# Optimization experiments

Measured on AMD Instinct MI355X. Metric: run time of the kernel, lower is better.

## Reference

```python
import jax, jax.numpy as jnp
import numpy as np

N_IN, N_REC, N_OUT = 512, 2048, 128
D_MAX = 4      # delays drawn from [0, D_MAX]; possible_delays = 1..D_MAX
DT = 0.001


@jax.custom_vjp
def spike(v):
    # SpikeFunc.forward: heaviside(v > 0)
    return (v > 0.0).astype(v.dtype)

def _spike_fwd(v):
    return spike(v), v

def _spike_bwd(v, g):
    # SpikeFunc.backward: grad passes through unchanged for v >= 0,
    # scaled by relu(1 + v) for v < 0
    return (g * jnp.where(v < 0.0, jnp.maximum(1.0 + v, 0.0), 1.0),)

spike.defvjp(_spike_fwd, _spike_bwd)


def setup_inputs() -> dict:
    key = jax.random.key(0)
    ks = jax.random.split(key, 6)
    B, T = 64, 250
    x = (jax.random.uniform(ks[0], (B, N_IN, T)) < 0.05).astype(jnp.float32)
    delays = jax.random.randint(ks[1], (N_REC, N_REC), 0, D_MAX + 1, dtype=jnp.int32)

    def kaiming_uniform(k, shape, fan):
        bound = float(np.sqrt(6.0 / fan))
        return jax.random.uniform(k, shape, minval=-bound, maxval=bound, dtype=jnp.float32)

    W_i = kaiming_uniform(ks[2], (N_REC, N_IN), N_REC)            # fan_out mode
    W_r = kaiming_uniform(ks[3], (N_REC, N_REC), N_REC) * 0.05    # scaled for stable dynamics
    W_o = kaiming_uniform(ks[4], (N_OUT, N_REC), N_REC)
    return {
        'input_spike_raster': x,
        'delays': delays,
        'W_i': W_i, 'W_r': W_r, 'W_o': W_o,
        'B_r': jnp.zeros((N_REC,), jnp.float32),
        'B_o': jnp.zeros((N_OUT,), jnp.float32),
        'tau_rec': jnp.full((1,), 0.2, jnp.float32),
        'tau_out': jnp.full((1,), 0.2, jnp.float32),
        'thr_rec': jnp.full((1,), 0.5, jnp.float32),
    }


def reference(input_spike_raster, delays, W_i, W_r, W_o, B_r, B_o, tau_rec, tau_out, thr_rec):
    rec_c = jnp.exp(-DT * 10.0 / tau_rec)   # (1,)
    out_c = jnp.exp(-DT * 10.0 / tau_out)   # (1,)
    d_vals = jnp.arange(1, D_MAX + 1)       # possible (nonzero) delays
    # W_r * delay_mask.T for each delay d -> (D, n_rec, n_rec)
    masks = (delays[None, :, :] == d_vals[:, None, None])
    Wd = W_r[None] * jnp.transpose(masks, (0, 2, 1)).astype(W_r.dtype)

    B, n_in, T = input_spike_raster.shape
    xs = jnp.transpose(input_spike_raster, (2, 0, 1))  # (T, B, n_in)
    buf0 = jnp.zeros((D_MAX, B, N_REC), W_r.dtype)     # buf[k] = spikes at t-1-k

    def step(carry, inp):
        mem_rec, mem_out, buf = carry
        t, x_t = inp
        cur = x_t @ W_i.T + B_r                               # (B, n_rec)
        # delay d contributes only if t > d (matches torch `if t > d`)
        valid = (t > d_vals).astype(cur.dtype)                # (D,)
        cur = cur + jnp.einsum('dbn,dmn->bm', buf * valid[:, None, None], Wd)
        mem_rec = mem_rec * rec_c + cur
        z = spike(mem_rec - thr_rec)
        mem_rec = mem_rec - z * thr_rec
        mem_out = mem_out * out_c + z @ W_o.T + B_o
        buf = jnp.concatenate([z[None], buf[:-1]], axis=0)
        return (mem_rec, mem_out, buf), z

    init = (jnp.zeros((B, N_REC), W_r.dtype), jnp.zeros((B, N_OUT), W_r.dtype), buf0)
    (_, mem_out, _), zs = jax.lax.scan(step, init, (jnp.arange(T), xs))
    # torch returns (mem_pot_out, stack(rec_spikes, dim=2)) -> (B, n_rec, T)
    return mem_out, jnp.transpose(zs, (1, 2, 0))
```

## Files before the change

kernel.cpp:

```cpp
#include <hip/hip_runtime.h>

#define NIN  512
#define NREC 2048
#define NOUT 128
#define BB   64
#define TT   250

#define OFF_WRT  0UL
#define OFF_DP2  16777216UL
#define OFF_WIT  17825792UL
#define OFF_WOT  22020096UL
#define OFF_MASK 23068672UL
#define OFF_G    27164672UL
#define OFF_CNT  28213248UL

__device__ __forceinline__ int decode_delay(int v) {
    if (v >= 0 && v <= 4) return v;
    const float f = __int_as_float(v);
    if (f >= 0.5f && f <= 4.5f) return (int)(f + 0.5f);
    return 0;
}
__device__ __forceinline__ int delay_like(int v) {
    if (v >= 0 && v <= 4) return 1;
    const float f = __int_as_float(v);
    return (f >= 0.5f && f <= 4.5f) ? 1 : 0;
}
__device__ __forceinline__ unsigned lane_rank(unsigned long long m) {
    unsigned r = __builtin_amdgcn_mbcnt_lo((unsigned)m, 0u);
    return __builtin_amdgcn_mbcnt_hi((unsigned)(m >> 32), r);
}

__global__ __launch_bounds__(256) void k_prep(
    const void* __restrict__ c4A, const void* __restrict__ c4B,
    const float* __restrict__ Wi, const float* __restrict__ Wo,
    float* __restrict__ WrT, unsigned* __restrict__ dP2,
    float* __restrict__ WiT, float* __restrict__ WoT)
{
    const int* iA = (const int*)c4A;
    const int* iB = (const int*)c4B;
    int cntA = 0, cntB = 0;
    for (int j = 0; j < 64; ++j) { cntA += delay_like(iA[j]); cntB += delay_like(iB[j]); }
    const int*   dl = (cntA >= cntB) ? iA : iB;
    const float* Wr = (cntA >= cntB) ? (const float*)c4B : (const float*)c4A;

    const int idx = blockIdx.x * 256 + threadIdx.x;
    if (idx < NREC * NREC) {
        const int n = idx >> 11, m = idx & 2047;
        const int d = decode_delay(dl[idx]);
        const float w = Wr[(size_t)m * NREC + n];
        WrT[idx] = (d == 0) ? 0.0f : w;
        if ((m & 15) == 0) {
            unsigned pw = 0;
            for (int j = 0; j < 16; ++j) {
                const int dj = decode_delay(dl[idx + j]);
                const unsigned e = (dj == 0) ? 0u : (unsigned)(dj - 1);
                pw |= e << (2 * j);
            }
            dP2[idx >> 4] = pw;
        }
    }
    if (idx < NIN * NREC) {
        const int i = idx >> 11, m = idx & 2047;
        WiT[idx] = Wi[(size_t)m * NIN + i];
    }
    if (idx < NREC * NOUT) {
        const int n = idx >> 7, o = idx & 127;
        WoT[idx] = Wo[(size_t)o * NREC + n];
    }
}

#define ACCEV(wf, ee) { const int dd = (int)(((ee) >> sh) & 3u);                \
    const double wd = (double)(wf);                                             \
    a0 += (dd == 0) ? wd : 0.0; a1 += (dd == 1) ? wd : 0.0;                     \
    a2 += (dd == 2) ? wd : 0.0; a3 += (dd == 3) ? wd : 0.0; }

#define LD1(nn, W, E) { const unsigned n_ = (nn);                               \
    W = WrT[(n_ << 11) | colu]; E = dP2[(n_ << 7) | c4i]; }

#define LOAD8M(base, P) {                                                       \
    const uint4 sv_ = *reinterpret_cast<const uint4*>(&slist[(base)]);          \
    LD1(sv_.x & 0xffffu, w##P##0, e##P##0) LD1(sv_.x >> 16, w##P##1, e##P##1)   \
    LD1(sv_.y & 0xffffu, w##P##2, e##P##2) LD1(sv_.y >> 16, w##P##3, e##P##3)   \
    LD1(sv_.z & 0xffffu, w##P##4, e##P##4) LD1(sv_.z >> 16, w##P##5, e##P##5)   \
    LD1(sv_.w & 0xffffu, w##P##6, e##P##6) LD1(sv_.w >> 16, w##P##7, e##P##7) }

#define ACCP(P) { ACCEV(w##P##0, e##P##0) ACCEV(w##P##1, e##P##1)               \
    ACCEV(w##P##2, e##P##2) ACCEV(w##P##3, e##P##3)                             \
    ACCEV(w##P##4, e##P##4) ACCEV(w##P##5, e##P##5)                             \
    ACCEV(w##P##6, e##P##6) ACCEV(w##P##7, e##P##7) }

__global__ __launch_bounds__(1024) void k_main(
    const float* __restrict__ x,
    const float* __restrict__ WrT,
    const unsigned* __restrict__ dP2,
    const float* __restrict__ WiT,
    const float* __restrict__ Br,
    const float* __restrict__ tau_rec, const float* __restrict__ tau_out,
    const float* __restrict__ thr_rec,
    unsigned* __restrict__ spikeMask, unsigned* __restrict__ cnt,
    double* __restrict__ g)
{
    __shared__ int icnt[8];
    __shared__ __align__(16) unsigned short ilist[NIN];
    __shared__ __align__(16) unsigned short slist[NREC];
    __shared__ int stot_s;
    __shared__ double aEx[512];
    __shared__ double cEx[512];

    const int gid = blockIdx.x;
    const int r8  = gid & 7, kk = gid >> 3;
    const int q   = r8 >> 1;
    const int b   = kk * 2 + (r8 & 1);
    const int tid  = threadIdx.x;
    const int half = tid >> 9;
    const int u    = tid & 511;
    const int w    = tid >> 6;
    const int lane = tid & 63;
    const int col  = q * 512 + u;
    const unsigned colu = (unsigned)col;
    const unsigned c4i  = colu >> 4;
    const int sh        = (col & 15) * 2;

    const double rec_c = exp(-0.01 / (double)tau_rec[0]);
    const double out_c = exp(-0.01 / (double)tau_out[0]);
    const double thr   = (double)thr_rec[0];
    const double br    = (double)Br[col];
    double mem = 0.0, gacc = 0.0;
    double a0 = 0.0, a1 = 0.0, a2 = 0.0, a3 = 0.0;

    const float* xb = x + (size_t)b * NIN * TT;
    const float* Wc = WiT + col;
    float xv = (half == 0) ? xb[(size_t)u * TT] : 0.f;

    for (int t = 0; t < TT; ++t) {
        const bool ihit = (xv != 0.f);
        const unsigned long long im = __ballot(ihit);
        if (w < 8 && lane == 0) icnt[w] = __popcll(im);
        float xvn = 0.f;
        if (half == 0 && t + 1 < TT) xvn = xb[(size_t)u * TT + (t + 1)];
        __syncthreads();
        int ioffw = 0, itot = 0;
#pragma unroll
        for (int j = 0; j < 8; ++j) { const int c = icnt[j]; if (j < w) ioffw += c; itot += c; }
        if (ihit) ilist[ioffw + lane_rank(im)] = (unsigned short)u;
        __syncthreads();
        int iHalf = ((itot >> 1) + 7) & ~7; if (iHalf > itot) iHalf = itot;
        const int ikb = half ? iHalf : 0;
        const int ike = half ? itot  : iHalf;
        double cin = 0.0;
        {
            int k = ikb;
            for (; k + 8 <= ike; k += 8) {
                const uint4 sv = *reinterpret_cast<const uint4*>(&ilist[k]);
                const float v0 = Wc[(sv.x & 0xffffu) << 11];
                const float v1 = Wc[(sv.x >> 16)     << 11];
                const float v2 = Wc[(sv.y & 0xffffu) << 11];
                const float v3 = Wc[(sv.y >> 16)     << 11];
                const float v4 = Wc[(sv.z & 0xffffu) << 11];
                const float v5 = Wc[(sv.z >> 16)     << 11];
                const float v6 = Wc[(sv.w & 0xffffu) << 11];
                const float v7 = Wc[(sv.w >> 16)     << 11];
                cin += (double)v0; cin += (double)v1; cin += (double)v2; cin += (double)v3;
                cin += (double)v4; cin += (double)v5; cin += (double)v6; cin += (double)v7;
            }
            for (; k < ike; ++k) cin += (double)Wc[(unsigned)ilist[k] << 11];
        }
        xv = xvn;

        if (t >= 2) {
            const unsigned* gmp = spikeMask + (size_t)((t - 1) * BB + b) * 64;
            if (tid == 0) {
                while (__hip_atomic_load(&cnt[(t - 1) * BB + b],
                                         __ATOMIC_ACQUIRE, __HIP_MEMORY_SCOPE_AGENT) < 4u)
                    __builtin_amdgcn_s_sleep(1);
            }
            __syncthreads();
            if (tid < 64) {
                const unsigned wv = __hip_atomic_load(&gmp[tid],
                                        __ATOMIC_RELAXED, __HIP_MEMORY_SCOPE_AGENT);
                const int zc = __popc(wv);
                int inc = zc;
#pragma unroll
                for (int s = 1; s < 64; s <<= 1) {
                    const int up = __shfl_up(inc, s, 64);
                    if (lane >= s) inc += up;
                }
                int off = inc - zc;
                if (lane == 63) stot_s = inc;
                unsigned bits = wv;
                while (bits) {
                    const int bp = __ffs(bits) - 1;
                    bits &= bits - 1;
                    slist[off++] = (unsigned short)(tid * 32 + bp);
                }
            }
            __syncthreads();
            const int stot = stot_s;
            int sHalf = ((stot >> 1) + 7) & ~7; if (sHalf > stot) sHalf = stot;
            const int kb = half ? sHalf : 0;
            const int ke = half ? stot  : sHalf;
            int k = kb;
            {
                float wA0, wA1, wA2, wA3, wA4, wA5, wA6, wA7;
                float wB0, wB1, wB2, wB3, wB4, wB5, wB6, wB7;
                float wC0, wC1, wC2, wC3, wC4, wC5, wC6, wC7;
                unsigned eA0, eA1, eA2, eA3, eA4, eA5, eA6, eA7;
                unsigned eB0, eB1, eB2, eB3, eB4, eB5, eB6, eB7;
                unsigned eC0, eC1, eC2, eC3, eC4, eC5, eC6, eC7;
                if (ke - kb >= 48) {
                    LOAD8M(kb, A) LOAD8M(kb + 8, B) LOAD8M(kb + 16, C)
                    for (k = kb; k + 48 <= ke; k += 24) {
                        ACCP(A) LOAD8M(k + 24, A)
                        ACCP(B) LOAD8M(k + 32, B)
                        ACCP(C) LOAD8M(k + 40, C)
                    }
                    ACCP(A) ACCP(B) ACCP(C)
                    k += 24;
                }
            }
            for (; k + 8 <= ke; k += 8) {
                const uint4 sv = *reinterpret_cast<const uint4*>(&slist[k]);
                const unsigned n0 = sv.x & 0xffffu, n1 = sv.x >> 16;
                const unsigned n2 = sv.y & 0xffffu, n3 = sv.y >> 16;
                const unsigned n4 = sv.z & 0xffffu, n5 = sv.z >> 16;
                const unsigned n6 = sv.w & 0xffffu, n7 = sv.w >> 16;
                const float w0 = WrT[(n0 << 11) | colu]; const unsigned e0 = dP2[(n0 << 7) | c4i];
                const float w1 = WrT[(n1 << 11) | colu]; const unsigned e1 = dP2[(n1 << 7) | c4i];
                const float w2 = WrT[(n2 << 11) | colu]; const unsigned e2 = dP2[(n2 << 7) | c4i];
                const float w3 = WrT[(n3 << 11) | colu]; const unsigned e3 = dP2[(n3 << 7) | c4i];
                const float w4 = WrT[(n4 << 11) | colu]; const unsigned e4 = dP2[(n4 << 7) | c4i];
                const float w5 = WrT[(n5 << 11) | colu]; const unsigned e5 = dP2[(n5 << 7) | c4i];
                const float w6 = WrT[(n6 << 11) | colu]; const unsigned e6 = dP2[(n6 << 7) | c4i];
                const float w7 = WrT[(n7 << 11) | colu]; const unsigned e7 = dP2[(n7 << 7) | c4i];
                ACCEV(w0, e0) ACCEV(w1, e1) ACCEV(w2, e2) ACCEV(w3, e3)
                ACCEV(w4, e4) ACCEV(w5, e5) ACCEV(w6, e6) ACCEV(w7, e7)
            }
            for (; k < ke; ++k) {
                const unsigned n0 = (unsigned)slist[k];
                const float w0 = WrT[(n0 << 11) | colu];
                const unsigned e0 = dP2[(n0 << 7) | c4i];
                ACCEV(w0, e0)
            }
        }

        if (half) { aEx[u] = a0; cEx[u] = cin; }
        __syncthreads();
        bool z = false;
        if (half == 0) {
            const double cur = (a0 + aEx[u]) + (cin + cEx[u]) + br;
            mem = mem * rec_c + cur;
            z = (mem - thr) > 0.0;
            if (z) mem -= thr;
            gacc = gacc * out_c + (z ? 1.0 : 0.0);
        }
        a0 = a1; a1 = a2; a2 = a3; a3 = 0.0;

        const unsigned long long mz = __ballot(z);
        unsigned* gm = spikeMask + (size_t)(t * BB + b) * 64;
        if (w < 8) {
            if (lane == 0)
                __hip_atomic_store(&gm[q * 16 + 2 * w], (unsigned)(mz & 0xFFFFFFFFu),
                                   __ATOMIC_RELAXED, __HIP_MEMORY_SCOPE_AGENT);
            if (lane == 32)
                __hip_atomic_store(&gm[q * 16 + 2 * w + 1], (unsigned)(mz >> 32),
                                   __ATOMIC_RELAXED, __HIP_MEMORY_SCOPE_AGENT);
        }
        __syncthreads();
        if (tid == 0)
            __hip_atomic_fetch_add(&cnt[t * BB + b], 1u,
                                   __ATOMIC_RELEASE, __HIP_MEMORY_SCOPE_AGENT);
    }

    if (half == 0) g[(size_t)b * NREC + col] = gacc;
}

__global__ __launch_bounds__(256) void k_memout(
    const double* __restrict__ g, const float* __restrict__ WoT,
    const float* __restrict__ Bo, const float* __restrict__ tau_out,
    float* __restrict__ mout)
{
    __shared__ double gs[NREC];
    const int b = blockIdx.x, tid = threadIdx.x;
#pragma unroll
    for (int k = 0; k < 8; ++k)
        gs[tid + 256 * k] = g[(size_t)b * NREC + tid + 256 * k];
    const double c = exp(-0.01 / (double)tau_out[0]);
    double S = 0.0;
    for (int t = 0; t < TT; ++t) S = S * c + 1.0;
    __syncthreads();
    if (tid < NOUT) {
        double a = 0.0;
        for (int n = 0; n < NREC; ++n)
            a += gs[n] * (double)WoT[n * NOUT + tid];
        a += (double)Bo[tid] * S;
        mout[(size_t)b * NOUT + tid] = (float)a;
    }
}

__global__ __launch_bounds__(256) void k_expand(
    const unsigned* __restrict__ spikeMask, float* __restrict__ zout)
{
    const int bid = blockIdx.x;
    const int b = bid >> 6, gw = bid & 63;
    const int t = threadIdx.x;
    if (t >= TT) return;
    const unsigned v = spikeMask[((size_t)(t * BB + b)) * 64 + gw];
    for (int j = 0; j < 32; ++j) {
        const int n = gw * 32 + j;
        zout[((size_t)b * NREC + n) * TT + t] = ((v >> j) & 1u) ? 1.0f : 0.0f;
    }
}

extern "C" void kernel_launch(void* const* d_in, const int* in_sizes, int n_in,
                              void* d_out, int out_size, void* d_ws, size_t ws_size,
                              hipStream_t stream) {
    const float *x = nullptr, *Wi = nullptr, *Wo = nullptr, *Br = nullptr, *Bo = nullptr;
    const void* c4[2] = {nullptr, nullptr};
    const float* sc[3] = {nullptr, nullptr, nullptr};
    int n4 = 0, nsc = 0;
    for (int i = 0; i < n_in; ++i) {
        switch (in_sizes[i]) {
            case 8192000: x  = (const float*)d_in[i]; break;
            case 1048576: Wi = (const float*)d_in[i]; break;
            case 262144:  Wo = (const float*)d_in[i]; break;
            case 2048:    Br = (const float*)d_in[i]; break;
            case 128:     Bo = (const float*)d_in[i]; break;
            case 4194304: if (n4 < 2)  c4[n4++]  = d_in[i]; break;
            case 1:       if (nsc < 3) sc[nsc++] = (const float*)d_in[i]; break;
            default: break;
        }
    }
    if (!x || !Wi || !Wo || !Br || !Bo || n4 < 2 || nsc < 3) {
        x  = (const float*)d_in[0];
        c4[0] = d_in[1];
        Wi = (const float*)d_in[2];
        c4[1] = d_in[3];
        Wo = (const float*)d_in[4];
        Br = (const float*)d_in[5];
        Bo = (const float*)d_in[6];
        sc[0] = (const float*)d_in[7];
        sc[1] = (const float*)d_in[8];
        sc[2] = (const float*)d_in[9];
    }
    const float* taur = sc[0];
    const float* tauo = sc[1];
    const float* thr  = sc[2];

    float* out = (float*)d_out;
    char* ws = (char*)d_ws;
    float*          WrT  = (float*)(ws + OFF_WRT);
    unsigned*       dP2  = (unsigned*)(ws + OFF_DP2);
    float*          WiT  = (float*)(ws + OFF_WIT);
    float*          WoT  = (float*)(ws + OFF_WOT);
    unsigned*       mask = (unsigned*)(ws + OFF_MASK);
    double*         g    = (double*)(ws + OFF_G);
    unsigned*       cnt  = (unsigned*)(ws + OFF_CNT);

    hipMemsetAsync(cnt, 0, (size_t)TT * BB * sizeof(unsigned), stream);
    hipLaunchKernelGGL(k_prep, dim3((NREC * NREC + 255) / 256), dim3(256), 0, stream,
                       c4[0], c4[1], Wi, Wo, WrT, dP2, WiT, WoT);
    hipLaunchKernelGGL(k_main, dim3(256), dim3(1024), 0, stream,
                       x, WrT, dP2, WiT, Br, taur, tauo, thr, mask, cnt, g);
    hipLaunchKernelGGL(k_memout, dim3(BB), dim3(256), 0, stream,
                       g, WoT, Bo, tauo, out);
    hipLaunchKernelGGL(k_expand, dim3(BB * 64), dim3(256), 0, stream,
                       mask, out + 8192);
}
```

Measured before the change: 4.227 ms.

## Stage spiking-row weights into LDS via global_load_lds in chunks

Replaces the per-thread register-pipelined gather of recurrent weight rows and delay codes with a chunked scheme. The 16 waves cooperatively copy up to CH spiking rows into shared memory using global_load_lds, then each thread accumulates from LDS. The intent is wider, coalesced row fetches that bypass registers, but it adds two block-wide barriers per chunk and drops the deep software prefetch, so load latency is no longer hidden behind compute. It also raises shared-memory use by about 90 KB per block.

```diff
diff --git a/kernel.cpp b/kernel.cpp
--- a/kernel.cpp
+++ b/kernel.cpp
@@ -5,6 +5,7 @@
 #define NOUT 128
 #define BB   64
 #define TT   250
+#define CH   40
 
 #define OFF_WRT  0UL
 #define OFF_DP2  16777216UL
@@ -74,20 +75,10 @@
     a0 += (dd == 0) ? wd : 0.0; a1 += (dd == 1) ? wd : 0.0;                     \
     a2 += (dd == 2) ? wd : 0.0; a3 += (dd == 3) ? wd : 0.0; }
 
-#define LD1(nn, W, E) { const unsigned n_ = (nn);                               \
-    W = WrT[(n_ << 11) | colu]; E = dP2[(n_ << 7) | c4i]; }
-
-#define LOAD8M(base, P) {                                                       \
-    const uint4 sv_ = *reinterpret_cast<const uint4*>(&slist[(base)]);          \
-    LD1(sv_.x & 0xffffu, w##P##0, e##P##0) LD1(sv_.x >> 16, w##P##1, e##P##1)   \
-    LD1(sv_.y & 0xffffu, w##P##2, e##P##2) LD1(sv_.y >> 16, w##P##3, e##P##3)   \
-    LD1(sv_.z & 0xffffu, w##P##4, e##P##4) LD1(sv_.z >> 16, w##P##5, e##P##5)   \
-    LD1(sv_.w & 0xffffu, w##P##6, e##P##6) LD1(sv_.w >> 16, w##P##7, e##P##7) }
-
-#define ACCP(P) { ACCEV(w##P##0, e##P##0) ACCEV(w##P##1, e##P##1)               \
-    ACCEV(w##P##2, e##P##2) ACCEV(w##P##3, e##P##3)                             \
-    ACCEV(w##P##4, e##P##4) ACCEV(w##P##5, e##P##5)                             \
-    ACCEV(w##P##6, e##P##6) ACCEV(w##P##7, e##P##7) }
+#define GLL(gp, lp, sz)                                                         \
+    __builtin_amdgcn_global_load_lds(                                           \
+        (const __attribute__((address_space(1))) void*)(gp),                    \
+        (__attribute__((address_space(3))) void*)(lp), sz, 0, 0)
 
 __global__ __launch_bounds__(1024) void k_main(
     const float* __restrict__ x,
@@ -106,20 +97,20 @@
     __shared__ int stot_s;
     __shared__ double aEx[512];
     __shared__ double cEx[512];
+    __shared__ __align__(16) float    wlds[CH][512];
+    __shared__ __align__(16) unsigned dlds[CH][64];
 
     const int gid = blockIdx.x;
-    const int r8  = gid & 7, kk = gid >> 3;
+    const int r8  = gid & 7, kk0 = gid >> 3;
     const int q   = r8 >> 1;
-    const int b   = kk * 2 + (r8 & 1);
+    const int b   = kk0 * 2 + (r8 & 1);
     const int tid  = threadIdx.x;
     const int half = tid >> 9;
     const int u    = tid & 511;
     const int w    = tid >> 6;
     const int lane = tid & 63;
     const int col  = q * 512 + u;
-    const unsigned colu = (unsigned)col;
-    const unsigned c4i  = colu >> 4;
-    const int sh        = (col & 15) * 2;
+    const int sh   = (col & 15) * 2;
 
     const double rec_c = exp(-0.01 / (double)tau_rec[0]);
     const double out_c = exp(-0.01 / (double)tau_out[0]);
@@ -199,47 +190,29 @@
             int sHalf = ((stot >> 1) + 7) & ~7; if (sHalf > stot) sHalf = stot;
             const int kb = half ? sHalf : 0;
             const int ke = half ? stot  : sHalf;
-            int k = kb;
-            {
-                float wA0, wA1, wA2, wA3, wA4, wA5, wA6, wA7;
-                float wB0, wB1, wB2, wB3, wB4, wB5, wB6, wB7;
-                float wC0, wC1, wC2, wC3, wC4, wC5, wC6, wC7;
-                unsigned eA0, eA1, eA2, eA3, eA4, eA5, eA6, eA7;
-                unsigned eB0, eB1, eB2, eB3, eB4, eB5, eB6, eB7;
-                unsigned eC0, eC1, eC2, eC3, eC4, eC5, eC6, eC7;
-                if (ke - kb >= 48) {
-                    LOAD8M(kb, A) LOAD8M(kb + 8, B) LOAD8M(kb + 16, C)
-                    for (k = kb; k + 48 <= ke; k += 24) {
-                        ACCP(A) LOAD8M(k + 24, A)
-                        ACCP(B) LOAD8M(k + 32, B)
-                        ACCP(C) LOAD8M(k + 40, C)
-                    }
-                    ACCP(A) ACCP(B) ACCP(C)
-                    k += 24;
+
+            for (int c0 = 0; c0 < stot; c0 += CH) {
+                int cend = c0 + CH; if (cend > stot) cend = stot;
+                for (int e = c0 + w; e < cend; e += 16) {
+                    const unsigned row = slist[e];
+                    const int slot = e - c0;
+                    const char* gA = (const char*)(WrT + ((row << 11) | (unsigned)(q * 512)))
+                                     + lane * 16;
+                    GLL(gA,        &wlds[slot][0],   16);
+                    GLL(gA + 1024, &wlds[slot][256], 16);
+                    const unsigned* dsrc = dP2 + ((row << 7) | (unsigned)(q * 32)) + (lane & 31);
+                    GLL(dsrc, &dlds[slot][0], 4);
                 }
-            }
-            for (; k + 8 <= ke; k += 8) {
-                const uint4 sv = *reinterpret_cast<const uint4*>(&slist[k]);
-                const unsigned n0 = sv.x & 0xffffu, n1 = sv.x >> 16;
-                const unsigned n2 = sv.y & 0xffffu, n3 = sv.y >> 16;
-                const unsigned n4 = sv.z & 0xffffu, n5 = sv.z >> 16;
-                const unsigned n6 = sv.w & 0xffffu, n7 = sv.w >> 16;
-                const float w0 = WrT[(n0 << 11) | colu]; const unsigned e0 = dP2[(n0 << 7) | c4i];
-                const float w1 = WrT[(n1 << 11) | colu]; const unsigned e1 = dP2[(n1 << 7) | c4i];
-                const float w2 = WrT[(n2 << 11) | colu]; const unsigned e2 = dP2[(n2 << 7) | c4i];
-                const float w3 = WrT[(n3 << 11) | colu]; const unsigned e3 = dP2[(n3 << 7) | c4i];
-                const float w4 = WrT[(n4 << 11) | colu]; const unsigned e4 = dP2[(n4 << 7) | c4i];
-                const float w5 = WrT[(n5 << 11) | colu]; const unsigned e5 = dP2[(n5 << 7) | c4i];
-                const float w6 = WrT[(n6 << 11) | colu]; const unsigned e6 = dP2[(n6 << 7) | c4i];
-                const float w7 = WrT[(n7 << 11) | colu]; const unsigned e7 = dP2[(n7 << 7) | c4i];
-                ACCEV(w0, e0) ACCEV(w1, e1) ACCEV(w2, e2) ACCEV(w3, e3)
-                ACCEV(w4, e4) ACCEV(w5, e5) ACCEV(w6, e6) ACCEV(w7, e7)
-            }
-            for (; k < ke; ++k) {
-                const unsigned n0 = (unsigned)slist[k];
-                const float w0 = WrT[(n0 << 11) | colu];
-                const unsigned e0 = dP2[(n0 << 7) | c4i];
-                ACCEV(w0, e0)
+                __syncthreads();
+                int lo = (kb > c0)  ? kb : c0;
+                int hi = (ke < cend) ? ke : cend;
+                for (int k = lo; k < hi; ++k) {
+                    const int slot = k - c0;
+                    const float    wf = wlds[slot][u];
+                    const unsigned ew = dlds[slot][u >> 4];
+                    ACCEV(wf, ew)
+                }
+                __syncthreads();
             }
         }
 
```

Result: slower. 4.540 ms (+7.4%).
